# Performance work log

Hardware: AMD Instinct MI355X
Metric: run time of the kernel (lower is better)

Reference implementation:

```python
import jax, jax.numpy as jnp
from jax import lax
import numpy as np

B, T, D, H = 64, 2048, 4, 256
ALPHA, WINDOW = 0.5, 64


def _make_binom(alpha, w):
    # (-1)^j * C(alpha, j) for j = 0..w (Grunwald-Letnikov coefficients)
    coeffs = []
    for j in range(w + 1):
        c = 1.0
        for i in range(j):
            c *= (alpha - i) / (i + 1)
        coeffs.append(((-1.0) ** j) * c)
    return jnp.asarray(np.array(coeffs, dtype=np.float32))


def setup_inputs() -> dict:
    key = jax.random.key(0)
    ks = jax.random.split(key, 12)
    x = jax.random.normal(ks[0], (B, T, D), dtype=jnp.float32)
    # time channel (index 3) must be monotonically increasing for time_diff**alpha
    time = jnp.arange(T, dtype=jnp.float32) * 0.1
    x = x.at[:, :, 3].set(jnp.broadcast_to(time, (B, T)))
    s = 0.05
    f32 = jnp.float32
    return {
        "x": x,
        "Wih0": s * jax.random.normal(ks[1], (H, D), f32),
        "Whh0": s * jax.random.normal(ks[2], (H, H), f32),
        "bih0": jnp.zeros((H,), f32),
        "bhh0": jnp.zeros((H,), f32),
        "Wih1": s * jax.random.normal(ks[3], (H, H), f32),
        "Whh1": s * jax.random.normal(ks[4], (H, H), f32),
        "bih1": jnp.zeros((H,), f32),
        "bhh1": jnp.zeros((H,), f32),
        "fcW": s * jax.random.normal(ks[5], (1, H), f32),
        "fcb": jnp.zeros((1,), f32),
        "Q": jnp.asarray(2.9, f32),
        "delta": jnp.asarray(1.0, f32),
        "f1W": s * jax.random.normal(ks[6], (H, 1), f32),
        "f1b": jnp.zeros((H,), f32),
        "f2W": s * jax.random.normal(ks[7], (1, H), f32),
        "f2b": jnp.zeros((1,), f32),
        "U0": jnp.asarray(1.0, f32),
        "R0": jnp.asarray(1.0, f32),
        "C1": jnp.asarray(1.0, f32),
        "R1": jnp.asarray(1.0, f32),
        "binom": _make_binom(ALPHA, WINDOW),
    }


def reference(x, Wih0, Whh0, bih0, bhh0, Wih1, Whh1, bih1, bhh1,
              fcW, fcb, Q, delta, f1W, f1b, f2W, f2b, U0, R0, C1, R1, binom):
    Bsz, Tlen, _ = x.shape

    def soc_fn(xx):
        xs = jnp.swapaxes(xx, 0, 1)  # [T, B, D]
        h0 = jnp.zeros((Bsz, Wih0.shape[0]), xx.dtype)

        def cell(Wih, Whh, bih, bhh):
            def f(h, xt):
                h = jnp.tanh(xt @ Wih.T + bih + h @ Whh.T + bhh)
                return h, h
            return f

        _, ys1 = lax.scan(cell(Wih0, Whh0, bih0, bhh0), h0, xs)  # [T, B, H]
        hT, _ = lax.scan(cell(Wih1, Whh1, bih1, bhh1), h0, ys1)  # [B, H]
        return hT @ fcW.T + fcb  # [B, 1]

    soc = soc_fn(x)
    # d soc / d x at last timestep, last feature (torch autograd.grad with ones grad_outputs)
    d_soc = jax.grad(lambda xx: soc_fn(xx).sum())(x)[:, -1, -1]  # [B]
    loss1 = delta / Q * x[:, -1, 1:2] + d_soc  # [B,1]+[B] -> [B,B] (matches torch broadcast)

    f_soc = (soc @ f1W.T + f1b) @ f2W.T + f2b  # [B, 1]

    # fractional-order windowed Up sequence (vectorized over t)
    v = x[:, :, 0]
    I = x[:, :, 1]
    time = x[:, :, 3]
    t_idx = jnp.arange(Tlen)
    start = jnp.maximum(0, t_idx - WINDOW + 1)
    valid = t_idx + 1 - start  # window length at each t
    tdiff = jnp.where(valid > 1,
                      (time - time[:, start]) / jnp.maximum(valid - 1, 1).astype(x.dtype),
                      jnp.asarray(1.0, x.dtype))  # [B, T]
    Ts = tdiff ** ALPHA
    # history_sum[t] = sum_{m=0}^{w-1} binom[w-m] * v[t-m] == causal conv with kernel binom[1:w+1]
    kern = binom[1:WINDOW + 1]
    hist = lax.conv_general_dilated(v[:, None, :], kern[None, None, :],
                                    (1,), [(WINDOW - 1, 0)])[:, 0, :]  # [B, T]
    Up = (-Ts / (R1 * C1)) * v + (Ts / C1) * I - hist  # [B, T]

    loss2 = f_soc - x[:, -1, 0:1] - R0 * x[:, -1, 1:2] - Up[:, -1]  # [B,1]-[B] -> [B,B]
    return (soc, loss1, loss2)
```

## Files before the change

### kernel.cpp

```cpp
#include <hip/hip_runtime.h>


#define TT 2048
#define HH 256
#define WIN 64

typedef uint uvec32 __attribute__((ext_vector_type(32)));

#if __has_builtin(__builtin_amdgcn_sdot4)
__device__ __forceinline__ int sdot4(uint a, uint b, int c) {
  return __builtin_amdgcn_sdot4((int)a, (int)b, c, false);
}
#else
__device__ __forceinline__ int sdot4(uint a, uint b, int c) {
#pragma unroll
  for (int k = 0; k < 4; ++k) {
    int av = (int)(a << (24 - 8 * k)) >> 24;
    int bv = (int)(b << (24 - 8 * k)) >> 24;
    c += av * bv;
  }
  return c;
}
#endif

__device__ __forceinline__ float tanh_fast(float x) {
  float xc = fminf(fmaxf(x, -15.f), 15.f);
  float e = __expf(2.f * xc);
  return (e - 1.f) * __builtin_amdgcn_rcpf(e + 1.f);
}

__device__ __forceinline__ float block_sum8(float v, float* red, int tid) {
#pragma unroll
  for (int off = 32; off >= 1; off >>= 1) v += __shfl_down(v, off, 64);
  __syncthreads();
  if ((tid & 63) == 0) red[tid >> 6] = v;
  __syncthreads();
  float s = 0.f;
#pragma unroll
  for (int w = 0; w < 8; ++w) s += red[w];
  return s;
}

__device__ __forceinline__ float max_half(const float* __restrict__ base) {
  const float4* g = (const float4*)base;
  float m = 0.f;
#pragma unroll
  for (int i = 0; i < 32; ++i) {
    float4 a = g[i];
    m = fmaxf(m, fmaxf(fmaxf(fabsf(a.x), fabsf(a.y)),
                       fmaxf(fabsf(a.z), fabsf(a.w))));
  }
  return m;
}

__device__ __forceinline__ uvec32 quant_half(const float* __restrict__ base,
                                             float inv) {
  uvec32 w;
  const float4* g = (const float4*)base;
#pragma unroll
  for (int i = 0; i < 32; ++i) {
    float4 a = g[i];
    int b0 = (int)rintf(a.x * inv), b1 = (int)rintf(a.y * inv);
    int b2 = (int)rintf(a.z * inv), b3 = (int)rintf(a.w * inv);
    w[i] = (uint)(b0 & 0xFF) | ((uint)(b1 & 0xFF) << 8) |
           ((uint)(b2 & 0xFF) << 16) | ((uint)(b3 & 0xFF) << 24);
  }
  return w;
}

__global__ __launch_bounds__(512) void rnn_chain_kernel(
    const float* __restrict__ x, const float* __restrict__ Wih0,
    const float* __restrict__ Whh0, const float* __restrict__ bih0,
    const float* __restrict__ bhh0, const float* __restrict__ Wih1,
    const float* __restrict__ Whh1, const float* __restrict__ bih1,
    const float* __restrict__ bhh1, const float* __restrict__ fcW,
    const float* __restrict__ fcb, const float* __restrict__ f1W,
    const float* __restrict__ f1b, const float* __restrict__ f2W,
    const float* __restrict__ f2b, const float* __restrict__ C1,
    const float* __restrict__ R1, const float* __restrict__ binom,
    float* __restrict__ out_soc,
    float* __restrict__ ws)
{
  const int b = blockIdx.x;
  const int tid = threadIdx.x;
  const int lane = tid & 63;
  const int wv = tid >> 6;
  const int half = lane >> 5;
  const int j = (wv << 5) | (lane & 31);

  __shared__ __align__(16) float xs[TT * 4];
  __shared__ __align__(16) uint qh0L[2][HH / 4];
  __shared__ __align__(16) uint qh1L[2][HH / 4];
  __shared__ float red[8];
  __shared__ float uL[HH];
  __shared__ float s0L[HH];
  __shared__ float pF[2 * HH];

  const float4* xg = (const float4*)(x + (size_t)b * TT * 4);
  float4* xl = (float4*)xs;
  for (int i = tid; i < TT; i += 512) xl[i] = xg[i];

  const size_t roff = (size_t)j * HH + half * 128;
  float mm0 = max_half(Whh0 + roff);
  float mm1 = max_half(Wih1 + roff);
  float mm2 = max_half(Whh1 + roff);
  const float m0 = fmaxf(mm0, __shfl_xor(mm0, 32));
  const float m1 = fmaxf(mm1, __shfl_xor(mm1, 32));
  const float m2 = fmaxf(mm2, __shfl_xor(mm2, 32));

  const uvec32 w0 = quant_half(Whh0 + roff, m0 > 0.f ? 127.f / m0 : 0.f);
  const uvec32 w1i = quant_half(Wih1 + roff, m1 > 0.f ? 127.f / m1 : 0.f);
  const uvec32 w1h = quant_half(Whh1 + roff, m2 > 0.f ? 127.f / m2 : 0.f);

  const float F0 = m0 * (1.f / 16129.f);
  const float F1i = m1 * (1.f / 16129.f);
  const float F1h = m2 * (1.f / 16129.f);
  const float4 wx = ((const float4*)Wih0)[j];
  const float bias0 = bih0[j] + bhh0[j];
  const float bias1 = bih1[j] + bhh1[j];

  __syncthreads();

  {
    float4 x0v = xl[0];
    float xd = wx.x * x0v.x + wx.y * x0v.y + wx.z * x0v.z + wx.w * x0v.w +
               bias0;
    float h00 = tanh_fast(xd);
    char* hb = half ? (char*)&qh1L[0][0] : (char*)&qh0L[0][0];
    char v = half ? (char)0 : (char)(int)rintf(h00 * 127.f);
    hb[j] = v;
  }
  __syncthreads();

  int cur = 0;
  float myh = 0.f;

  for (int t = 0; t < TT - 1; ++t) {
    const uint4* h0p = (const uint4*)&qh0L[cur][0] + half * 8;
    const uint4* h1p = (const uint4*)&qh1L[cur][0] + half * 8;
    int C = 0, E = 0, A = 0;
#pragma unroll
    for (int i = 0; i < 8; ++i) {
      uint4 u = h1p[i];
      C = sdot4(w1h[4 * i + 0], u.x, C);
      C = sdot4(w1h[4 * i + 1], u.y, C);
      C = sdot4(w1h[4 * i + 2], u.z, C);
      C = sdot4(w1h[4 * i + 3], u.w, C);
    }
#pragma unroll
    for (int i = 0; i < 8; ++i) {
      uint4 u = h0p[i];
      E = sdot4(w1i[4 * i + 0], u.x, E);
      A = sdot4(w0[4 * i + 0], u.x, A);
      E = sdot4(w1i[4 * i + 1], u.y, E);
      A = sdot4(w0[4 * i + 1], u.y, A);
      E = sdot4(w1i[4 * i + 2], u.z, E);
      A = sdot4(w0[4 * i + 2], u.z, A);
      E = sdot4(w1i[4 * i + 3], u.w, E);
      A = sdot4(w0[4 * i + 3], u.w, A);
    }
    A += __shfl_xor(A, 32);
    E += __shfl_xor(E, 32);
    C += __shfl_xor(C, 32);
    float4 xt = xl[t + 1];
    float xd = wx.x * xt.x + wx.y * xt.y + wx.z * xt.z + wx.w * xt.w + bias0;
    float z = half ? (F1i * (float)E + F1h * (float)C + bias1)
                   : (F0 * (float)A + xd);
    myh = tanh_fast(z);
    char* hb = half ? (char*)&qh1L[cur ^ 1][0] : (char*)&qh0L[cur ^ 1][0];
    hb[j] = (char)(int)rintf(myh * 127.f);
    cur ^= 1;
    __syncthreads();
  }

  {
    const uint4* h0p = (const uint4*)&qh0L[cur][0] + half * 8;
    const uint4* h1p = (const uint4*)&qh1L[cur][0] + half * 8;
    int C = 0, E = 0;
#pragma unroll
    for (int i = 0; i < 8; ++i) {
      uint4 u = h1p[i];
      C = sdot4(w1h[4 * i + 0], u.x, C);
      C = sdot4(w1h[4 * i + 1], u.y, C);
      C = sdot4(w1h[4 * i + 2], u.z, C);
      C = sdot4(w1h[4 * i + 3], u.w, C);
    }
#pragma unroll
    for (int i = 0; i < 8; ++i) {
      uint4 u = h0p[i];
      E = sdot4(w1i[4 * i + 0], u.x, E);
      E = sdot4(w1i[4 * i + 1], u.y, E);
      E = sdot4(w1i[4 * i + 2], u.z, E);
      E = sdot4(w1i[4 * i + 3], u.w, E);
    }
    E += __shfl_xor(E, 32);
    C += __shfl_xor(C, 32);
    if (half) myh = tanh_fast(F1i * (float)E + F1h * (float)C + bias1);
  }

  const float fw = fcW[j];

  float socb = block_sum8(half ? fw * myh : 0.f, red, tid) + fcb[0];
  if (tid == 0) out_soc[b] = socb;

  float fsv = half ? f2W[j] * (socb * f1W[j] + f1b[j]) : 0.f;
  float fsb = block_sum8(fsv, red, tid) + f2b[0];
  if (tid == 0) ws[64 + b] = fsb;

  if (half) uL[j] = fw * (1.f - myh * myh);
  else      s0L[j] = (1.f - myh * myh) * wx.w;
  __syncthreads();
  {
    const int h = tid & 255;
    const int kh = tid >> 8;
    float g = 0.f;
    const int k0 = kh * 128;
#pragma unroll 8
    for (int k = 0; k < 128; ++k)
      g += uL[k0 + k] * Wih1[(size_t)(k0 + k) * HH + h];
    pF[kh * HH + h] = g;
  }
  __syncthreads();
  float dsv = 0.f;
  if (tid < HH) dsv = (pF[tid] + pF[HH + tid]) * s0L[tid];
  float dsoc = block_sum8(dsv, red, tid);
  if (tid == 0) ws[b] = dsoc;

  float histv = 0.f;
  if (tid < WIN) histv = binom[tid + 1] * xs[(TT - WIN + tid) * 4 + 0];
  float hist = block_sum8(histv, red, tid);
  if (tid == 0) {
    float tl = xs[(TT - 1) * 4 + 3], t0v = xs[(TT - WIN) * 4 + 3];
    float tdiff = (tl - t0v) * (1.0f / (float)(WIN - 1));
    float Ts = sqrtf(tdiff);
    float vlast = xs[(TT - 1) * 4 + 0], Ilast = xs[(TT - 1) * 4 + 1];
    float r1 = R1[0], c1v = C1[0];
    float up = -Ts / (r1 * c1v) * vlast + Ts / c1v * Ilast - hist;
    ws[128 + b] = up;
  }
}

__global__ void assemble_kernel(const float* __restrict__ x,
                                const float* __restrict__ Q,
                                const float* __restrict__ delta,
                                const float* __restrict__ R0,
                                const float* __restrict__ ws,
                                float* __restrict__ out) {
  const int i = blockIdx.x;
  const int jj = threadIdx.x;
  const float dq = delta[0] / Q[0];
  const size_t base = ((size_t)i * TT + (TT - 1)) * 4;
  const float xv0 = x[base + 0];
  const float xv1 = x[base + 1];
  const float fs = ws[64 + i];
  out[64 + i * 64 + jj] = dq * xv1 + ws[jj];
  out[64 + 4096 + i * 64 + jj] = fs - xv0 - R0[0] * xv1 - ws[128 + jj];
}

extern "C" void kernel_launch(void* const* d_in, const int* in_sizes, int n_in,
                              void* d_out, int out_size, void* d_ws,
                              size_t ws_size, hipStream_t stream) {
  const float* x    = (const float*)d_in[0];
  const float* Wih0 = (const float*)d_in[1];
  const float* Whh0 = (const float*)d_in[2];
  const float* bih0 = (const float*)d_in[3];
  const float* bhh0 = (const float*)d_in[4];
  const float* Wih1 = (const float*)d_in[5];
  const float* Whh1 = (const float*)d_in[6];
  const float* bih1 = (const float*)d_in[7];
  const float* bhh1 = (const float*)d_in[8];
  const float* fcW  = (const float*)d_in[9];
  const float* fcb  = (const float*)d_in[10];
  const float* Q    = (const float*)d_in[11];
  const float* delta= (const float*)d_in[12];
  const float* f1W  = (const float*)d_in[13];
  const float* f1b  = (const float*)d_in[14];
  const float* f2W  = (const float*)d_in[15];
  const float* f2b  = (const float*)d_in[16];
  const float* R0   = (const float*)d_in[18];
  const float* C1   = (const float*)d_in[19];
  const float* R1   = (const float*)d_in[20];
  const float* binom= (const float*)d_in[21];

  float* out = (float*)d_out;
  float* ws  = (float*)d_ws;

  hipLaunchKernelGGL(rnn_chain_kernel, dim3(64), dim3(512), 0, stream, x,
                     Wih0, Whh0, bih0, bhh0, Wih1, Whh1, bih1, bhh1, fcW, fcb,
                     f1W, f1b, f2W, f2b, C1, R1, binom, out, ws);
  hipLaunchKernelGGL(assemble_kernel, dim3(64), dim3(64), 0, stream, x, Q,
                     delta, R0, ws, out);
}
```

Before: 1.617 ms.

## Split hidden-state K halves across waves and broadcast inputs via readlane

```diff
diff --git a/kernel.cpp b/kernel.cpp
--- a/kernel.cpp
+++ b/kernel.cpp
@@ -21,6 +21,12 @@
   }
   return c;
 }
+#endif
+
+#if __has_builtin(__builtin_amdgcn_readlane)
+#define RL(v, l) ((uint)__builtin_amdgcn_readlane((int)(v), (l)))
+#else
+#define RL(v, l) ((uint)__shfl((int)(v), (l), 64))
 #endif
 
 __device__ __forceinline__ float tanh_fast(float x) {
@@ -85,12 +91,15 @@
   const int tid = threadIdx.x;
   const int lane = tid & 63;
   const int wv = tid >> 6;
-  const int half = lane >> 5;
-  const int j = (wv << 5) | (lane & 31);
+  const int half = wv >> 2;
+  const int wrow = ((wv & 3) << 6) | lane;
 
   __shared__ __align__(16) float xs[TT * 4];
-  __shared__ __align__(16) uint qh0L[2][HH / 4];
-  __shared__ __align__(16) uint qh1L[2][HH / 4];
+  __shared__ __align__(16) uint qh[2][128];
+  __shared__ int pA[HH];
+  __shared__ int pE[HH];
+  __shared__ int pC[HH];
+  __shared__ float sM[3][2][HH];
   __shared__ float red[8];
   __shared__ float uL[HH];
   __shared__ float s0L[HH];
@@ -100,13 +109,14 @@
   float4* xl = (float4*)xs;
   for (int i = tid; i < TT; i += 512) xl[i] = xg[i];
 
-  const size_t roff = (size_t)j * HH + half * 128;
-  float mm0 = max_half(Whh0 + roff);
-  float mm1 = max_half(Wih1 + roff);
-  float mm2 = max_half(Whh1 + roff);
-  const float m0 = fmaxf(mm0, __shfl_xor(mm0, 32));
-  const float m1 = fmaxf(mm1, __shfl_xor(mm1, 32));
-  const float m2 = fmaxf(mm2, __shfl_xor(mm2, 32));
+  const size_t roff = (size_t)wrow * HH + half * 128;
+  sM[0][half][wrow] = max_half(Whh0 + roff);
+  sM[1][half][wrow] = max_half(Wih1 + roff);
+  sM[2][half][wrow] = max_half(Whh1 + roff);
+  __syncthreads();
+  const float m0 = fmaxf(sM[0][0][wrow], sM[0][1][wrow]);
+  const float m1 = fmaxf(sM[1][0][wrow], sM[1][1][wrow]);
+  const float m2 = fmaxf(sM[2][0][wrow], sM[2][1][wrow]);
 
   const uvec32 w0 = quant_half(Whh0 + roff, m0 > 0.f ? 127.f / m0 : 0.f);
   const uvec32 w1i = quant_half(Wih1 + roff, m1 > 0.f ? 127.f / m1 : 0.f);
@@ -115,100 +125,90 @@
   const float F0 = m0 * (1.f / 16129.f);
   const float F1i = m1 * (1.f / 16129.f);
   const float F1h = m2 * (1.f / 16129.f);
-  const float4 wx = ((const float4*)Wih0)[j];
-  const float bias0 = bih0[j] + bhh0[j];
-  const float bias1 = bih1[j] + bhh1[j];
+  const float4 wx = ((const float4*)Wih0)[wrow];
+  const float bias0 = bih0[wrow] + bhh0[wrow];
+  const float bias1 = bih1[wrow] + bhh1[wrow];
 
   __syncthreads();
 
   {
     float4 x0v = xl[0];
-    float xd = wx.x * x0v.x + wx.y * x0v.y + wx.z * x0v.z + wx.w * x0v.w +
-               bias0;
-    float h00 = tanh_fast(xd);
-    char* hb = half ? (char*)&qh1L[0][0] : (char*)&qh0L[0][0];
-    char v = half ? (char)0 : (char)(int)rintf(h00 * 127.f);
-    hb[j] = v;
-  }
-  __syncthreads();
+    if (half == 0) {
+      float xd = wx.x * x0v.x + wx.y * x0v.y + wx.z * x0v.z + wx.w * x0v.w +
+                 bias0;
+      ((char*)&qh[0][0])[wrow] = (char)(int)rintf(tanh_fast(xd) * 127.f);
+    } else {
+      ((char*)&qh[0][0])[256 + wrow] = (char)0;
+    }
+  }
+  __syncthreads();
+
+  const int didx = (half << 5) + (lane & 31) + ((lane >> 5) << 6);
 
   int cur = 0;
   float myh = 0.f;
 
   for (int t = 0; t < TT - 1; ++t) {
-    const uint4* h0p = (const uint4*)&qh0L[cur][0] + half * 8;
-    const uint4* h1p = (const uint4*)&qh1L[cur][0] + half * 8;
-    int C = 0, E = 0, A = 0;
-#pragma unroll
-    for (int i = 0; i < 8; ++i) {
-      uint4 u = h1p[i];
-      C = sdot4(w1h[4 * i + 0], u.x, C);
-      C = sdot4(w1h[4 * i + 1], u.y, C);
-      C = sdot4(w1h[4 * i + 2], u.z, C);
-      C = sdot4(w1h[4 * i + 3], u.w, C);
-    }
-#pragma unroll
-    for (int i = 0; i < 8; ++i) {
-      uint4 u = h0p[i];
-      E = sdot4(w1i[4 * i + 0], u.x, E);
-      A = sdot4(w0[4 * i + 0], u.x, A);
-      E = sdot4(w1i[4 * i + 1], u.y, E);
-      A = sdot4(w0[4 * i + 1], u.y, A);
-      E = sdot4(w1i[4 * i + 2], u.z, E);
-      A = sdot4(w0[4 * i + 2], u.z, A);
-      E = sdot4(w1i[4 * i + 3], u.w, E);
-      A = sdot4(w0[4 * i + 3], u.w, A);
-    }
-    A += __shfl_xor(A, 32);
-    E += __shfl_xor(E, 32);
-    C += __shfl_xor(C, 32);
-    float4 xt = xl[t + 1];
-    float xd = wx.x * xt.x + wx.y * xt.y + wx.z * xt.z + wx.w * xt.w + bias0;
-    float z = half ? (F1i * (float)E + F1h * (float)C + bias1)
-                   : (F0 * (float)A + xd);
-    myh = tanh_fast(z);
-    char* hb = half ? (char*)&qh1L[cur ^ 1][0] : (char*)&qh0L[cur ^ 1][0];
-    hb[j] = (char)(int)rintf(myh * 127.f);
+    const uint hw = qh[cur][didx];
+    int A = 0, E = 0, C = 0;
+#pragma unroll
+    for (int i = 0; i < 32; ++i) {
+      uint s0 = RL(hw, i);
+      A = sdot4(w0[i], s0, A);
+      E = sdot4(w1i[i], s0, E);
+      uint s1 = RL(hw, 32 + i);
+      C = sdot4(w1h[i], s1, C);
+    }
+    if (half == 1) pA[wrow] = A;
+    else { pE[wrow] = E; pC[wrow] = C; }
+    __syncthreads();
+    if (half == 0) {
+      float4 xt = xl[t + 1];
+      float xd = wx.x * xt.x + wx.y * xt.y + wx.z * xt.z + wx.w * xt.w +
+                 bias0;
+      int At = A + pA[wrow];
+      myh = tanh_fast(F0 * (float)At + xd);
+      ((char*)&qh[cur ^ 1][0])[wrow] = (char)(int)rintf(myh * 127.f);
+    } else {
+      int Et = E + pE[wrow];
+      int Ct = C + pC[wrow];
+      myh = tanh_fast(F1i * (float)Et + F1h * (float)Ct + bias1);
+      ((char*)&qh[cur ^ 1][0])[256 + wrow] = (char)(int)rintf(myh * 127.f);
+    }
     cur ^= 1;
     __syncthreads();
   }
 
   {
-    const uint4* h0p = (const uint4*)&qh0L[cur][0] + half * 8;
-    const uint4* h1p = (const uint4*)&qh1L[cur][0] + half * 8;
-    int C = 0, E = 0;
-#pragma unroll
-    for (int i = 0; i < 8; ++i) {
-      uint4 u = h1p[i];
-      C = sdot4(w1h[4 * i + 0], u.x, C);
-      C = sdot4(w1h[4 * i + 1], u.y, C);
-      C = sdot4(w1h[4 * i + 2], u.z, C);
-      C = sdot4(w1h[4 * i + 3], u.w, C);
-    }
-#pragma unroll
-    for (int i = 0; i < 8; ++i) {
-      uint4 u = h0p[i];
-      E = sdot4(w1i[4 * i + 0], u.x, E);
-      E = sdot4(w1i[4 * i + 1], u.y, E);
-      E = sdot4(w1i[4 * i + 2], u.z, E);
-      E = sdot4(w1i[4 * i + 3], u.w, E);
-    }
-    E += __shfl_xor(E, 32);
-    C += __shfl_xor(C, 32);
-    if (half) myh = tanh_fast(F1i * (float)E + F1h * (float)C + bias1);
-  }
-
-  const float fw = fcW[j];
+    const uint hw = qh[cur][didx];
+    int E = 0, C = 0;
+#pragma unroll
+    for (int i = 0; i < 32; ++i) {
+      uint s0 = RL(hw, i);
+      E = sdot4(w1i[i], s0, E);
+      uint s1 = RL(hw, 32 + i);
+      C = sdot4(w1h[i], s1, C);
+    }
+    if (half == 0) { pE[wrow] = E; pC[wrow] = C; }
+    __syncthreads();
+    if (half == 1) {
+      int Et = E + pE[wrow];
+      int Ct = C + pC[wrow];
+      myh = tanh_fast(F1i * (float)Et + F1h * (float)Ct + bias1);
+    }
+  }
+
+  const float fw = fcW[wrow];
 
   float socb = block_sum8(half ? fw * myh : 0.f, red, tid) + fcb[0];
   if (tid == 0) out_soc[b] = socb;
 
-  float fsv = half ? f2W[j] * (socb * f1W[j] + f1b[j]) : 0.f;
+  float fsv = half ? f2W[wrow] * (socb * f1W[wrow] + f1b[wrow]) : 0.f;
   float fsb = block_sum8(fsv, red, tid) + f2b[0];
   if (tid == 0) ws[64 + b] = fsb;
 
-  if (half) uL[j] = fw * (1.f - myh * myh);
-  else      s0L[j] = (1.f - myh * myh) * wx.w;
+  if (half) uL[wrow] = fw * (1.f - myh * myh);
+  else      s0L[wrow] = (1.f - myh * myh) * wx.w;
   __syncthreads();
   {
     const int h = tid & 255;
```

Result: slower. 2.061 ms (+27.5%).
